# Optimization experiments

Hardware: AMD Instinct MI355X
Metric: run time of the kernel (lower is better)

## Reference

```python
import jax, jax.numpy as jnp
import numpy as np

HIDDEN = 1024
N_EMB = 4096
K_TOP = 64
EPS = 1e-6


def rmsnorm(x, w):
    xf = x.astype(jnp.float32)
    y = xf * jax.lax.rsqrt(jnp.mean(xf * xf, axis=-1, keepdims=True) + EPS)
    return y.astype(x.dtype) * w


def setup_inputs() -> dict:
    key = jax.random.key(0)
    ks = jax.random.split(key, 5)
    B, S, D, N = 16, 2048, HIDDEN, N_EMB
    bound = 1.0 / np.sqrt(D)  # torch Linear reset_parameters uniform bound
    return {
        "X": jax.random.normal(ks[0], (B, S, D), dtype=jnp.float32),
        "alpha": jnp.zeros((), dtype=jnp.float32),
        "E": jax.random.normal(ks[1], (N, D), dtype=jnp.float32) / np.sqrt(D),
        "Wq": jax.random.uniform(ks[2], (D, D), dtype=jnp.float32, minval=-bound, maxval=bound),
        "Wk": jax.random.uniform(ks[3], (D, D), dtype=jnp.float32, minval=-bound, maxval=bound),
        "xn_w": jnp.ones((D,), dtype=jnp.float32),
        "sn_w": jnp.ones((D,), dtype=jnp.float32),
        "on_w": jnp.ones((D,), dtype=jnp.float32),
    }


def reference(X, alpha, E, Wq, Wk, xn_w, sn_w, on_w):
    scale = HIDDEN ** (-0.5)
    Xn = rmsnorm(X, xn_w)            # (B,S,D)
    En = rmsnorm(E, sn_w)            # (N,D)
    Q = Xn @ Wq.T                    # (B,S,D)
    Km = En @ Wk.T                   # (N,D)
    scores = jnp.einsum('bsd,nd->bsn', Q, Km) * scale  # (B,S,N)
    global_scores = jnp.max(scores, axis=1)            # (B,N)
    top_vals, _ = jax.lax.top_k(global_scores, K_TOP)
    cutoff = top_vals[:, -1:]                          # (B,1)
    masked = jnp.where(global_scores >= cutoff, global_scores, -jnp.inf)
    dense_w = jax.nn.softmax(global_scores, axis=-1)
    sparse_w = jax.nn.softmax(masked, axis=-1)
    weights = alpha * dense_w + (1.0 - alpha) * sparse_w  # (B,N)
    O = rmsnorm(weights @ En, on_w)                      # (B,D)
    return O, weights
```

## Files before the change

kernel.cpp:

```cpp
#include <hip/hip_runtime.h>


namespace {

constexpr int D_DIM = 1024;
constexpr int NE    = 4096;
constexpr int BATCH = 16;
constexpr int SEQ   = 2048;
constexpr int MX    = BATCH * SEQ;
constexpr int KTOP  = 64;
constexpr int CAND  = 128;
constexpr int BK    = 32;

using f32x4  = __attribute__((ext_vector_type(4))) float;
using bf16x8 = __attribute__((ext_vector_type(8))) short;
using i32x4  = __attribute__((ext_vector_type(4))) int;

__device__ inline unsigned encf(float f) {
  unsigned u = __float_as_uint(f);
  return (u & 0x80000000u) ? ~u : (u | 0x80000000u);
}
__device__ inline float decf(unsigned e) {
  unsigned u = (e & 0x80000000u) ? (e ^ 0x80000000u) : ~e;
  return __uint_as_float(u);
}

__device__ inline unsigned short f2bf(float f) {
  unsigned u = __float_as_uint(f);
  unsigned lsb = (u >> 16) & 1u;
  u += 0x7fffu + lsb;
  return (unsigned short)(u >> 16);
}
__device__ inline float bf2f(unsigned short h) {
  return __uint_as_float(((unsigned)h) << 16);
}

__device__ inline void gload16(const void* gsrc, void* ldst) {
  __builtin_amdgcn_global_load_lds(
      (const __attribute__((address_space(1))) unsigned int*)gsrc,
      (__attribute__((address_space(3))) unsigned int*)ldst, 16, 0, 0);
}

__global__ void row_rinv_k(const float* __restrict__ X, float* __restrict__ rinv) {
  __shared__ float l4[4];
  int row = blockIdx.x;
  float4 v = ((const float4*)(X + (size_t)row * D_DIM))[threadIdx.x];
  float ss = v.x * v.x + v.y * v.y + v.z * v.z + v.w * v.w;
  for (int o = 32; o > 0; o >>= 1) ss += __shfl_xor(ss, o);
  int lane = threadIdx.x & 63, w = threadIdx.x >> 6;
  if (lane == 0) l4[w] = ss;
  __syncthreads();
  if (threadIdx.x == 0) {
    float t = l4[0] + l4[1] + l4[2] + l4[3];
    rinv[row] = rsqrtf(t * (1.0f / D_DIM) + 1e-6f);
  }
}

__global__ void rinv_quantx_k(const float* __restrict__ X, float* __restrict__ rinv,
                              float* __restrict__ sxr, int* __restrict__ XQ,
                              unsigned* __restrict__ gmax) {
  __shared__ float l4[4], m4[4];
  int row = blockIdx.x;
  if (row < 256) gmax[row * 256 + threadIdx.x] = 0u;
  float4 v = ((const float4*)(X + (size_t)row * D_DIM))[threadIdx.x];
  float ss = v.x * v.x + v.y * v.y + v.z * v.z + v.w * v.w;
  float am = fmaxf(fmaxf(fabsf(v.x), fabsf(v.y)), fmaxf(fabsf(v.z), fabsf(v.w)));
  for (int o = 32; o > 0; o >>= 1) {
    ss += __shfl_xor(ss, o);
    am = fmaxf(am, __shfl_xor(am, o));
  }
  int lane = threadIdx.x & 63, w = threadIdx.x >> 6;
  if (lane == 0) { l4[w] = ss; m4[w] = am; }
  __syncthreads();
  float t  = l4[0] + l4[1] + l4[2] + l4[3];
  float amax = fmaxf(fmaxf(m4[0], m4[1]), fmaxf(m4[2], m4[3]));
  amax = fmaxf(amax, 1e-30f);
  float ri = rsqrtf(t * (1.0f / D_DIM) + 1e-6f);
  if (threadIdx.x == 0) {
    rinv[row] = ri;
    sxr[row]  = ri * amax * (1.0f / 127.0f);
  }
  float qs = 127.0f / amax;
  int q0 = (int)rintf(v.x * qs) & 0xff;
  int q1 = (int)rintf(v.y * qs) & 0xff;
  int q2 = (int)rintf(v.z * qs) & 0xff;
  int q3 = (int)rintf(v.w * qs) & 0xff;
  XQ[(size_t)row * 256 + threadIdx.x] = q0 | (q1 << 8) | (q2 << 16) | (q3 << 24);
}

__global__ void prep_w_k(const float* __restrict__ Wq, const float* __restrict__ Wk,
                         const float* __restrict__ cw, float* __restrict__ T,
                         unsigned short* __restrict__ H, unsigned short* __restrict__ L) {
  __shared__ float t[32][33], u[32][33];
  int k0 = blockIdx.x * 32, d0 = blockIdx.y * 32;
  int tx = threadIdx.x & 31, ty4 = (threadIdx.x >> 5) * 4;
#pragma unroll
  for (int i = 0; i < 4; ++i) {
    t[ty4 + i][tx] = Wq[(size_t)(d0 + ty4 + i) * D_DIM + k0 + tx];
    u[ty4 + i][tx] = Wk[(size_t)(d0 + ty4 + i) * D_DIM + k0 + tx];
  }
  __syncthreads();
#pragma unroll
  for (int i = 0; i < 4; ++i) {
    int a = ty4 + i;
    T[(size_t)(k0 + a) * D_DIM + d0 + tx] = t[tx][a];
    float v = u[tx][a] * cw[k0 + a];
    unsigned short h = f2bf(v);
    H[(size_t)(k0 + a) * D_DIM + d0 + tx] = h;
    L[(size_t)(k0 + a) * D_DIM + d0 + tx] = f2bf(v - bf2f(h));
  }
}

template <int KLEN>
__global__ __launch_bounds__(256, 2) void gemm_a32_part_k(
    const float* __restrict__ A, const float* __restrict__ rinv,
    const unsigned short* __restrict__ BH, const unsigned short* __restrict__ BL,
    float* __restrict__ Of) {
  __shared__ __align__(16) float lA[128 * 32];
  __shared__ __align__(16) unsigned short lBH[128 * 32];
  __shared__ __align__(16) unsigned short lBL[128 * 32];
  __shared__ float ldsR[128];

  int tid = threadIdx.x;
  int lane = tid & 63, wid = tid >> 6;
  int wr = wid >> 1, wc = wid & 1;
  int fr = lane & 15, fg = lane >> 4;
  long m0 = (long)blockIdx.x * 128;
  long n0 = (long)blockIdx.y * 128;
  int kbeg = blockIdx.z * KLEN;
  float* Op = Of + (size_t)blockIdx.z * ((size_t)gridDim.x * 128 * D_DIM);

  if (tid < 128) ldsR[tid] = rinv ? rinv[m0 + tid] : 1.0f;

  f32x4 acc[4][4] = {};

  for (int kk = kbeg; kk < kbeg + KLEN; kk += BK) {
#pragma unroll
    for (int i = 0; i < 4; ++i) {
      int chunk = i * 256 + tid;
      int r = chunk >> 3, c = chunk & 7;
      int cs = c ^ (r & 7);
      const float* src = A + (m0 + r) * (long)D_DIM + kk + cs * 4;
      gload16(src, (void*)(lA + ((i * 256 + (tid & ~63)) << 2)));
    }
#pragma unroll
    for (int i = 0; i < 2; ++i) {
      int chunk = i * 256 + tid;
      int r = chunk >> 2, c = chunk & 3;
      int cs = c ^ ((r >> 1) & 3);
      long boff = (n0 + r) * (long)D_DIM + kk + cs * 8;
      int lo = (i * 256 + (tid & ~63)) << 3;
      gload16(BH + boff, (void*)(lBH + lo));
      gload16(BL + boff, (void*)(lBL + lo));
    }
    __syncthreads();

    bf16x8 aH[4], aL[4], bH[4], bL[4];
#pragma unroll
    for (int m = 0; m < 4; ++m) {
      int row = wr * 64 + m * 16 + fr;
      int rm = row & 7;
      f32x4 p0 = *(const f32x4*)(lA + row * 32 + (((fg * 2 + 0) ^ rm) * 4));
      f32x4 p1 = *(const f32x4*)(lA + row * 32 + (((fg * 2 + 1) ^ rm) * 4));
#pragma unroll
      for (int e = 0; e < 8; ++e) {
        float f = (e < 4) ? p0[e] : p1[e - 4];
        unsigned short h = f2bf(f);
        aH[m][e] = (short)h;
        aL[m][e] = (short)f2bf(f - bf2f(h));
      }
    }
#pragma unroll
    for (int n = 0; n < 4; ++n) {
      int row = wc * 64 + n * 16 + fr;
      int sc = fg ^ ((row >> 1) & 3);
      bH[n] = *(const bf16x8*)(lBH + row * 32 + sc * 8);
      bL[n] = *(const bf16x8*)(lBL + row * 32 + sc * 8);
    }
#pragma unroll
    for (int m = 0; m < 4; ++m)
#pragma unroll
      for (int n = 0; n < 4; ++n) {
        acc[m][n] = __builtin_amdgcn_mfma_f32_16x16x32_bf16(aH[m], bH[n], acc[m][n], 0, 0, 0);
        acc[m][n] = __builtin_amdgcn_mfma_f32_16x16x32_bf16(aH[m], bL[n], acc[m][n], 0, 0, 0);
        acc[m][n] = __builtin_amdgcn_mfma_f32_16x16x32_bf16(aL[m], bH[n], acc[m][n], 0, 0, 0);
      }
    __syncthreads();
  }

#pragma unroll
  for (int m = 0; m < 4; ++m) {
#pragma unroll
    for (int j = 0; j < 4; ++j) {
      int rloc = wr * 64 + m * 16 + fg * 4 + j;
      float rv = ldsR[rloc];
      long grow = m0 + rloc;
#pragma unroll
      for (int n = 0; n < 4; ++n) {
        long gcol = n0 + wc * 64 + n * 16 + fr;
        Op[grow * D_DIM + gcol] = acc[m][n][j] * rv;
      }
    }
  }
}

__global__ void sum_split_w2_k(const float* __restrict__ P0, const float* __restrict__ P1,
                               const float* __restrict__ P2, const float* __restrict__ P3,
                               unsigned short* __restrict__ H, unsigned short* __restrict__ L) {
  size_t i4 = ((size_t)blockIdx.x * 256 + threadIdx.x) * 4;
  float4 a = *(const float4*)(P0 + i4);
  float4 b = *(const float4*)(P1 + i4);
  float4 c = *(const float4*)(P2 + i4);
  float4 d = *(const float4*)(P3 + i4);
  float v[4] = {a.x + b.x + c.x + d.x, a.y + b.y + c.y + d.y,
                a.z + b.z + c.z + d.z, a.w + b.w + c.w + d.w};
  unsigned short h[4], l[4];
#pragma unroll
  for (int i = 0; i < 4; ++i) {
    h[i] = f2bf(v[i]);
    l[i] = f2bf(v[i] - bf2f(h[i]));
  }
  *(ushort4*)(H + i4) = make_ushort4(h[0], h[1], h[2], h[3]);
  *(ushort4*)(L + i4) = make_ushort4(l[0], l[1], l[2], l[3]);
}

__global__ void sum_split_p_k(const float* __restrict__ P0, const float* __restrict__ P1,
                              unsigned short* __restrict__ PH, unsigned short* __restrict__ PL,
                              float* __restrict__ sp, int* __restrict__ PQ) {
  __shared__ float m4[4];
  int row = blockIdx.x, tid = threadIdx.x;
  size_t i4 = (size_t)row * D_DIM + tid * 4;
  float4 a = *(const float4*)(P0 + i4);
  float4 b = *(const float4*)(P1 + i4);
  float v0 = a.x + b.x, v1 = a.y + b.y, v2 = a.z + b.z, v3 = a.w + b.w;
  unsigned short h0 = f2bf(v0), h1 = f2bf(v1), h2 = f2bf(v2), h3 = f2bf(v3);
  *(ushort4*)(PH + i4) = make_ushort4(h0, h1, h2, h3);
  *(ushort4*)(PL + i4) = make_ushort4(f2bf(v0 - bf2f(h0)), f2bf(v1 - bf2f(h1)),
                                      f2bf(v2 - bf2f(h2)), f2bf(v3 - bf2f(h3)));
  float am = fmaxf(fmaxf(fabsf(v0), fabsf(v1)), fmaxf(fabsf(v2), fabsf(v3)));
  for (int o = 32; o > 0; o >>= 1) am = fmaxf(am, __shfl_xor(am, o));
  int lane = tid & 63, w = tid >> 6;
  if (lane == 0) m4[w] = am;
  __syncthreads();
  float amax = fmaxf(fmaxf(m4[0], m4[1]), fmaxf(m4[2], m4[3]));
  amax = fmaxf(amax, 1e-30f);
  if (tid == 0) sp[row] = amax * (1.0f / 127.0f);
  float qs = 127.0f / amax;
  int q0 = (int)rintf(v0 * qs) & 0xff;
  int q1 = (int)rintf(v1 * qs) & 0xff;
  int q2 = (int)rintf(v2 * qs) & 0xff;
  int q3 = (int)rintf(v3 * qs) & 0xff;
  PQ[(size_t)row * 256 + tid] = q0 | (q1 << 8) | (q2 << 16) | (q3 << 24);
}

__global__ __launch_bounds__(512, 4) void gemm_scores1_k(
    const signed char* __restrict__ XQ, const signed char* __restrict__ PQ,
    const float* __restrict__ sxr, const float* __restrict__ sp,
    unsigned* __restrict__ gmax) {
  __shared__ __align__(16) signed char lA[3][128 * 64];
  __shared__ __align__(16) signed char lB[3][256 * 64];
  __shared__ float ldsR[128];

  int tid = threadIdx.x;
  int lane = tid & 63, wid = tid >> 6;
  int wwr = wid >> 2;
  int wwc = wid & 3;
  int fr = lane & 15, fg = lane >> 4;

  int id = blockIdx.x;
  int xcd = id & 7;
  int r = id >> 3;
  int tile_n = (r & 7) | ((r >> 8) << 3);
  int tile_m = xcd * 32 + ((r >> 3) & 31);
  long m0 = (long)tile_m * 128;
  long n0 = (long)tile_n * 256;

  if (tid < 128) ldsR[tid] = sxr[m0 + tid];

  auto stageTile = [&](int buf, int kt) {
    int kk = kt * 64;
    {
      int r2 = tid >> 2, c = tid & 3;
      int cs = c ^ ((r2 >> 1) & 3);
      gload16(XQ + (m0 + r2) * (long)D_DIM + kk + cs * 16,
              (void*)(&lA[buf][0] + ((tid & ~63) << 4)));
    }
#pragma unroll
    for (int i = 0; i < 2; ++i) {
      int chunk = i * 512 + tid;
      int r2 = chunk >> 2, c = chunk & 3;
      int cs = c ^ ((r2 >> 1) & 3);
      gload16(PQ + (n0 + r2) * (long)D_DIM + kk + cs * 16,
              (void*)(&lB[buf][0] + ((i * 512 + (tid & ~63)) << 4)));
    }
  };

  i32x4 acc[4][4] = {};

  stageTile(0, 0);
  stageTile(1, 1);
  asm volatile("s_waitcnt lgkmcnt(0)" ::: "memory");

#pragma unroll
  for (int kt = 0; kt < 16; ++kt) {
    const int cur = kt % 3;
    const int nxt = (kt + 2) % 3;
    const signed char* As = &lA[cur][0];
    const signed char* Bs = &lB[cur][0];

    if (kt < 15) {
      asm volatile("s_waitcnt vmcnt(3)" ::: "memory");
    } else {
      asm volatile("s_waitcnt vmcnt(0)" ::: "memory");
    }
    __builtin_amdgcn_s_barrier();
    if (kt + 2 < 16) stageTile(nxt, kt + 2);

    i32x4 aF[4], bF[4];
#pragma unroll
    for (int mi = 0; mi < 4; ++mi) {
      int row = wwr * 64 + mi * 16 + fr;
      int ck = fg ^ ((row >> 1) & 3);
      aF[mi] = *(const i32x4*)(As + row * 64 + ck * 16);
    }
#pragma unroll
    for (int ni = 0; ni < 4; ++ni) {
      int row = wwc * 64 + ni * 16 + fr;
      int ck = fg ^ ((row >> 1) & 3);
      bF[ni] = *(const i32x4*)(Bs + row * 64 + ck * 16);
    }
    __builtin_amdgcn_s_setprio(1);
#pragma unroll
    for (int mi = 0; mi < 4; ++mi)
#pragma unroll
      for (int ni = 0; ni < 4; ++ni)
        acc[mi][ni] = __builtin_amdgcn_mfma_i32_16x16x64_i8(
            aF[mi], bF[ni], acc[mi][ni], 0, 0, 0);
    __builtin_amdgcn_s_setprio(0);
  }

  int b = (int)(m0 >> 11);
#pragma unroll
  for (int ni = 0; ni < 4; ++ni) {
    long col = n0 + wwc * 64 + ni * 16 + fr;
    float spc = sp[col];
    float v = -3.0e38f;
#pragma unroll
    for (int mi = 0; mi < 4; ++mi)
#pragma unroll
      for (int j = 0; j < 4; ++j) {
        int row = wwr * 64 + mi * 16 + fg * 4 + j;
        v = fmaxf(v, (float)acc[mi][ni][j] * ldsR[row]);
      }
    v *= spc;
    v = fmaxf(v, __shfl_xor(v, 16));
    v = fmaxf(v, __shfl_xor(v, 32));
    if (fg == 0) {
      atomicMax(&gmax[(long)b * NE + col], encf(v * 0.03125f));
    }
  }
}

__global__ void cand_select_k(const unsigned* __restrict__ gmax,
                              int* __restrict__ candIdx, unsigned* __restrict__ gmax2) {
  __shared__ unsigned enc[NE];
  __shared__ int ic[257];
  int tid = threadIdx.x;
  int lane = tid & 63, w = tid >> 6;
  int zb = blockIdx.x;
  if (tid < CAND) gmax2[zb * CAND + tid] = 0u;
  const unsigned* g = gmax + (size_t)zb * NE;
  for (int i = tid; i < NE; i += 256) enc[i] = g[i];
  __syncthreads();

  unsigned cur = 0;
  for (int bit = 31; bit >= 0; --bit) {
    unsigned cand = cur | (1u << bit);
    int c = 0;
    for (int i = tid; i < NE; i += 256) c += (enc[i] >= cand) ? 1 : 0;
    for (int o = 32; o > 0; o >>= 1) c += __shfl_xor(c, o);
    __syncthreads();
    if (lane == 0) ic[w] = c;
    __syncthreads();
    int tot = ic[0] + ic[1] + ic[2] + ic[3];
    if (tot >= CAND) cur = cand;
    if (tot == CAND) break;
  }

  int myc = 0;
  for (int i = tid; i < NE; i += 256) myc += (enc[i] >= cur) ? 1 : 0;
  __syncthreads();
  ic[tid] = myc;
  __syncthreads();
  if (tid == 0) {
    int s = 0;
    for (int t = 0; t < 256; ++t) { int v = ic[t]; ic[t] = s; s += v; }
  }
  __syncthreads();
  int off = ic[tid];
  for (int i = tid; i < NE; i += 256)
    if (enc[i] >= cur) {
      if (off < CAND) candIdx[zb * CAND + off] = i;
      ++off;
    }
}

__global__ __launch_bounds__(256, 2) void gemm_rescore_k(
    const float* __restrict__ X, const float* __restrict__ rinvA,
    const unsigned short* __restrict__ PH, const unsigned short* __restrict__ PL,
    const int* __restrict__ candIdx, unsigned* __restrict__ gmax2) {
  __shared__ __align__(16) float lA[128 * 32];
  __shared__ __align__(16) unsigned short lBH[128 * 32], lBL[128 * 32];
  __shared__ float ldsR[128];

  int tid = threadIdx.x;
  int lane = tid & 63, wid = tid >> 6;
  int wr = wid >> 1, wc = wid & 1;
  int fr = lane & 15, fg = lane >> 4;
  int z = blockIdx.z;
  long m0 = (long)blockIdx.x * 128;
  long arow0 = (long)z * SEQ + m0;

  if (tid < 128) ldsR[tid] = rinvA[arow0 + tid];

  long bbase[2];
#pragma unroll
  for (int i = 0; i < 2; ++i) {
    int r = (i * 256 + tid) >> 2;
    bbase[i] = (long)candIdx[z * CAND + r] * D_DIM;
  }

  f32x4 acc[4][4] = {};

  for (int kk = 0; kk < D_DIM; kk += BK) {
#pragma unroll
    for (int i = 0; i < 4; ++i) {
      int chunk = i * 256 + tid;
      int r = chunk >> 3, c = chunk & 7;
      int cs = c ^ (r & 7);
      const float* src = X + (arow0 + r) * (long)D_DIM + kk + cs * 4;
      gload16(src, (void*)(lA + ((i * 256 + (tid & ~63)) << 2)));
    }
#pragma unroll
    for (int i = 0; i < 2; ++i) {
      int chunk = i * 256 + tid;
      int c = chunk & 3;
      int r = chunk >> 2;
      int cs = c ^ ((r >> 1) & 3);
      long boff = bbase[i] + kk + cs * 8;
      int lo = (i * 256 + (tid & ~63)) << 3;
      gload16(PH + boff, (void*)(lBH + lo));
      gload16(PL + boff, (void*)(lBL + lo));
    }
    __syncthreads();

    bf16x8 aH[4], aL[4], bH[4], bL[4];
#pragma unroll
    for (int m = 0; m < 4; ++m) {
      int row = wr * 64 + m * 16 + fr;
      int rm = row & 7;
      f32x4 p0 = *(const f32x4*)(lA + row * 32 + (((fg * 2 + 0) ^ rm) * 4));
      f32x4 p1 = *(const f32x4*)(lA + row * 32 + (((fg * 2 + 1) ^ rm) * 4));
#pragma unroll
      for (int e = 0; e < 8; ++e) {
        float f = (e < 4) ? p0[e] : p1[e - 4];
        unsigned short h = f2bf(f);
        aH[m][e] = (short)h;
        aL[m][e] = (short)f2bf(f - bf2f(h));
      }
    }
#pragma unroll
    for (int n = 0; n < 4; ++n) {
      int row = wc * 64 + n * 16 + fr;
      int sc = fg ^ ((row >> 1) & 3);
      bH[n] = *(const bf16x8*)(lBH + row * 32 + sc * 8);
      bL[n] = *(const bf16x8*)(lBL + row * 32 + sc * 8);
    }
#pragma unroll
    for (int m = 0; m < 4; ++m)
#pragma unroll
      for (int n = 0; n < 4; ++n) {
        acc[m][n] = __builtin_amdgcn_mfma_f32_16x16x32_bf16(aH[m], bH[n], acc[m][n], 0, 0, 0);
        acc[m][n] = __builtin_amdgcn_mfma_f32_16x16x32_bf16(aH[m], bL[n], acc[m][n], 0, 0, 0);
        acc[m][n] = __builtin_amdgcn_mfma_f32_16x16x32_bf16(aL[m], bH[n], acc[m][n], 0, 0, 0);
      }
    __syncthreads();
  }

#pragma unroll
  for (int n = 0; n < 4; ++n) {
    float v = -3.0e38f;
#pragma unroll
    for (int m = 0; m < 4; ++m)
#pragma unroll
      for (int j = 0; j < 4; ++j) {
        float rv = ldsR[wr * 64 + m * 16 + fg * 4 + j];
        v = fmaxf(v, acc[m][n][j] * rv);
      }
    v = fmaxf(v, __shfl_xor(v, 16));
    v = fmaxf(v, __shfl_xor(v, 32));
    if (fg == 0) {
      int col = wc * 64 + n * 16 + fr;
      atomicMax(&gmax2[z * CAND + col], encf(v * 0.03125f));
    }
  }
}

__global__ void final_k(const unsigned* __restrict__ gmax,
                        const unsigned* __restrict__ gmax2,
                        const int* __restrict__ candIdx,
                        const float* __restrict__ alpha_p,
                        const float* __restrict__ E, const float* __restrict__ rinvE,
                        const float* __restrict__ sn_w, const float* __restrict__ on_w,
                        float* __restrict__ wout, float* __restrict__ O) {
  __shared__ unsigned enc[NE];
  __shared__ int sel[NE];
  __shared__ unsigned ubc[4];
  __shared__ float l4[4];
  __shared__ int ic[257];
  int tid = threadIdx.x;
  int lane = tid & 63, w = tid >> 6;
  int b = blockIdx.x;
  const unsigned* g = gmax + (size_t)b * NE;
  for (int i = tid; i < NE; i += 256) enc[i] = g[i];
  __syncthreads();
  if (tid < CAND) enc[candIdx[b * CAND + tid]] = gmax2[b * CAND + tid];
  __syncthreads();

  unsigned mx = 0;
  for (int i = tid; i < NE; i += 256) mx = enc[i] > mx ? enc[i] : mx;
  for (int o = 32; o > 0; o >>= 1) {
    unsigned other = (unsigned)__shfl_xor((int)mx, o);
    if (other > mx) mx = other;
  }
  if (lane == 0) ubc[w] = mx;
  __syncthreads();
  unsigned m1e = ubc[0];
  for (int t = 1; t < 4; ++t) m1e = ubc[t] > m1e ? ubc[t] : m1e;
  float m1 = decf(m1e);

  unsigned cur = 0;
  for (int bit = 31; bit >= 0; --bit) {
    unsigned cand = cur | (1u << bit);
    int c = 0;
    for (int i = tid; i < NE; i += 256) c += (enc[i] >= cand) ? 1 : 0;
    for (int o = 32; o > 0; o >>= 1) c += __shfl_xor(c, o);
    __syncthreads();
    if (lane == 0) ic[w] = c;
    __syncthreads();
    int tot = ic[0] + ic[1] + ic[2] + ic[3];
    if (tot >= KTOP) cur = cand;
    if (tot == KTOP) break;
  }

  float sd = 0.f, ssum = 0.f;
  for (int i = tid; i < NE; i += 256) {
    float e = expf(decf(enc[i]) - m1);
    sd += e;
    if (enc[i] >= cur) ssum += e;
  }
  for (int o = 32; o > 0; o >>= 1) { sd += __shfl_xor(sd, o); ssum += __shfl_xor(ssum, o); }
  __syncthreads();
  if (lane == 0) { l4[w] = sd; }
  __syncthreads();
  float SD = l4[0] + l4[1] + l4[2] + l4[3];
  __syncthreads();
  if (lane == 0) { l4[w] = ssum; }
  __syncthreads();
  float SS = l4[0] + l4[1] + l4[2] + l4[3];

  float alpha = alpha_p[0];
  float wd = alpha / SD;
  float ws_ = (1.0f - alpha) / SS;
  for (int i = tid; i < NE; i += 256) {
    float e = expf(decf(enc[i]) - m1);
    float wv = wd * e + ((enc[i] >= cur) ? ws_ * e : 0.0f);
    wout[(size_t)b * NE + i] = wv;
  }

  int myc = 0;
  for (int i = tid; i < NE; i += 256) myc += (enc[i] >= cur) ? 1 : 0;
  __syncthreads();
  ic[tid] = myc;
  __syncthreads();
  if (tid == 0) {
    int s = 0;
    for (int t = 0; t < 256; ++t) { int v = ic[t]; ic[t] = s; s += v; }
    ic[256] = s;
  }
  __syncthreads();
  int off = ic[tid];
  for (int i = tid; i < NE; i += 256)
    if (enc[i] >= cur) sel[off++] = i;
  __syncthreads();
  int nsel = ic[256];

  float acc[4] = {0.f, 0.f, 0.f, 0.f};
  if (alpha == 0.0f) {
    float coef = wd + ws_;
    for (int j = 0; j < nsel; ++j) {
      int n = sel[j];
      float e = expf(decf(enc[n]) - m1);
      float wv = coef * e * rinvE[n];
      const float* er = E + (size_t)n * D_DIM;
#pragma unroll
      for (int i = 0; i < 4; ++i) acc[i] += wv * er[tid + 256 * i];
    }
  } else {
    for (int n = 0; n < NE; ++n) {
      float e = expf(decf(enc[n]) - m1);
      float wv = (wd * e + ((enc[n] >= cur) ? ws_ * e : 0.0f)) * rinvE[n];
      const float* er = E + (size_t)n * D_DIM;
#pragma unroll
      for (int i = 0; i < 4; ++i) acc[i] += wv * er[tid + 256 * i];
    }
  }
  float ssq = 0.f;
#pragma unroll
  for (int i = 0; i < 4; ++i) {
    acc[i] *= sn_w[tid + 256 * i];
    ssq += acc[i] * acc[i];
  }
  for (int o = 32; o > 0; o >>= 1) ssq += __shfl_xor(ssq, o);
  if (lane == 0) l4[w] = ssq;
  __syncthreads();
  float tot = l4[0] + l4[1] + l4[2] + l4[3];
  float rn = rsqrtf(tot * (1.0f / D_DIM) + 1e-6f);
#pragma unroll
  for (int i = 0; i < 4; ++i)
    O[(size_t)b * D_DIM + tid + 256 * i] = acc[i] * rn * on_w[tid + 256 * i];
}

}

extern "C" void kernel_launch(void* const* d_in, const int* in_sizes, int n_in,
                              void* d_out, int out_size, void* d_ws, size_t ws_size,
                              hipStream_t stream) {
  const float* X     = (const float*)d_in[0];
  const float* alpha = (const float*)d_in[1];
  const float* E     = (const float*)d_in[2];
  const float* Wq    = (const float*)d_in[3];
  const float* Wk    = (const float*)d_in[4];
  const float* xn_w  = (const float*)d_in[5];
  const float* sn_w  = (const float*)d_in[6];
  const float* on_w  = (const float*)d_in[7];
  float* O    = (float*)d_out;
  float* Wout = (float*)d_out + (size_t)BATCH * D_DIM;

  char* ws = (char*)d_ws;
  size_t off = 0;
  auto alloc = [&](size_t bytes) {
    char* p = ws + off;
    off += (bytes + 255) & ~(size_t)255;
    return p;
  };
  signed char*    XQ    = (signed char*)alloc((size_t)MX * D_DIM);
  signed char*    PQ    = (signed char*)alloc((size_t)NE * D_DIM);
  float*          WqTf  = (float*)alloc((size_t)D_DIM * D_DIM * 4);
  unsigned short* WkTH  = (unsigned short*)alloc((size_t)D_DIM * D_DIM * 2);
  unsigned short* WkTL  = (unsigned short*)alloc((size_t)D_DIM * D_DIM * 2);
  unsigned short* W2TH  = (unsigned short*)alloc((size_t)D_DIM * D_DIM * 2);
  unsigned short* W2TL  = (unsigned short*)alloc((size_t)D_DIM * D_DIM * 2);
  unsigned short* PH    = (unsigned short*)alloc((size_t)NE * D_DIM * 2);
  unsigned short* PL    = (unsigned short*)alloc((size_t)NE * D_DIM * 2);
  float*          W2p   = (float*)alloc((size_t)4 * D_DIM * D_DIM * 4);
  float*          Pp    = (float*)alloc((size_t)2 * NE * D_DIM * 4);
  float* rinvX = (float*)alloc((size_t)MX * 4);
  float* sxr   = (float*)alloc((size_t)MX * 4);
  float* rinvE = (float*)alloc((size_t)NE * 4);
  float* sp    = (float*)alloc((size_t)NE * 4);
  unsigned* gmax  = (unsigned*)alloc((size_t)BATCH * NE * 4);
  unsigned* gmax2 = (unsigned*)alloc((size_t)BATCH * CAND * 4);
  int* candIdx = (int*)alloc((size_t)BATCH * CAND * 4);
  if (off > ws_size) return;

  row_rinv_k<<<NE, 256, 0, stream>>>(E, rinvE);
  prep_w_k<<<dim3(D_DIM / 32, D_DIM / 32), 256, 0, stream>>>(
      Wq, Wk, sn_w, WqTf, WkTH, WkTL);
  gemm_a32_part_k<256><<<dim3(8, 8, 4), 256, 0, stream>>>(
      WqTf, xn_w, WkTH, WkTL, W2p);
  sum_split_w2_k<<<D_DIM * D_DIM / 1024, 256, 0, stream>>>(
      W2p, W2p + (size_t)D_DIM * D_DIM, W2p + (size_t)2 * D_DIM * D_DIM,
      W2p + (size_t)3 * D_DIM * D_DIM, W2TH, W2TL);
  gemm_a32_part_k<512><<<dim3(NE / 128, D_DIM / 128, 2), 256, 0, stream>>>(
      E, rinvE, W2TH, W2TL, Pp);
  sum_split_p_k<<<NE, 256, 0, stream>>>(
      Pp, Pp + (size_t)NE * D_DIM, PH, PL, sp, (int*)PQ);

  rinv_quantx_k<<<MX, 256, 0, stream>>>(X, rinvX, sxr, (int*)XQ, gmax);
  gemm_scores1_k<<<(MX / 128) * (NE / 256), 512, 0, stream>>>(XQ, PQ, sxr, sp, gmax);

  cand_select_k<<<BATCH, 256, 0, stream>>>(gmax, candIdx, gmax2);
  gemm_rescore_k<<<dim3(SEQ / 128, 1, BATCH), 256, 0, stream>>>(
      X, rinvX, PH, PL, candIdx, gmax2);
  final_k<<<BATCH, 256, 0, stream>>>(gmax, gmax2, candIdx, alpha, E, rinvE,
                                     sn_w, on_w, Wout, O);
}
```

Before: 375.7 us.

## Fold candidate selection into rescore and final kernels, dropping cand_select launch

Removes the separate cand_select_k launch. Each gemm_rescore_k block (16 per batch) and final_k now recompute the radix-select of the 128 candidates from gmax in LDS. gmax2 zeroing moves into rinv_quantx_k. This saves one kernel launch and its serialization gap, at the cost of redundant selection work in every rescore block and 16KB of extra LDS, which may reduce occupancy of the rescore GEMM.

After: 390.7 us. +4.0%, slower.

```diff
diff --git a/kernel.cpp b/kernel.cpp
--- a/kernel.cpp
+++ b/kernel.cpp
@@ -41,6 +41,42 @@
       (__attribute__((address_space(3))) unsigned int*)ldst, 16, 0, 0);
 }
 
+__device__ inline unsigned derive_cands(const unsigned* enc, int* ic,
+                                        int* candL, int tid) {
+  int lane = tid & 63, w = tid >> 6;
+  unsigned cur = 0;
+  for (int bit = 31; bit >= 0; --bit) {
+    unsigned cand = cur | (1u << bit);
+    int c = 0;
+    for (int i = tid; i < NE; i += 256) c += (enc[i] >= cand) ? 1 : 0;
+    for (int o = 32; o > 0; o >>= 1) c += __shfl_xor(c, o);
+    __syncthreads();
+    if (lane == 0) ic[w] = c;
+    __syncthreads();
+    int tot = ic[0] + ic[1] + ic[2] + ic[3];
+    if (tot >= CAND) cur = cand;
+    if (tot == CAND) break;
+  }
+  int myc = 0;
+  for (int i = tid; i < NE; i += 256) myc += (enc[i] >= cur) ? 1 : 0;
+  __syncthreads();
+  ic[tid] = myc;
+  __syncthreads();
+  if (tid == 0) {
+    int s = 0;
+    for (int t = 0; t < 256; ++t) { int v = ic[t]; ic[t] = s; s += v; }
+  }
+  __syncthreads();
+  int off = ic[tid];
+  for (int i = tid; i < NE; i += 256)
+    if (enc[i] >= cur) {
+      if (off < CAND) candL[off] = i;
+      ++off;
+    }
+  __syncthreads();
+  return cur;
+}
+
 __global__ void row_rinv_k(const float* __restrict__ X, float* __restrict__ rinv) {
   __shared__ float l4[4];
   int row = blockIdx.x;
@@ -58,10 +94,11 @@
 
 __global__ void rinv_quantx_k(const float* __restrict__ X, float* __restrict__ rinv,
                               float* __restrict__ sxr, int* __restrict__ XQ,
-                              unsigned* __restrict__ gmax) {
+                              unsigned* __restrict__ gmax, unsigned* __restrict__ gmax2) {
   __shared__ float l4[4], m4[4];
   int row = blockIdx.x;
   if (row < 256) gmax[row * 256 + threadIdx.x] = 0u;
+  else if (row < 264) gmax2[(row - 256) * 256 + threadIdx.x] = 0u;
   float4 v = ((const float4*)(X + (size_t)row * D_DIM))[threadIdx.x];
   float ss = v.x * v.x + v.y * v.y + v.z * v.z + v.w * v.w;
   float am = fmaxf(fmaxf(fabsf(v.x), fabsf(v.y)), fmaxf(fabsf(v.z), fabsf(v.w)));
@@ -361,57 +398,16 @@
   }
 }
 
-__global__ void cand_select_k(const unsigned* __restrict__ gmax,
-                              int* __restrict__ candIdx, unsigned* __restrict__ gmax2) {
-  __shared__ unsigned enc[NE];
-  __shared__ int ic[257];
-  int tid = threadIdx.x;
-  int lane = tid & 63, w = tid >> 6;
-  int zb = blockIdx.x;
-  if (tid < CAND) gmax2[zb * CAND + tid] = 0u;
-  const unsigned* g = gmax + (size_t)zb * NE;
-  for (int i = tid; i < NE; i += 256) enc[i] = g[i];
-  __syncthreads();
-
-  unsigned cur = 0;
-  for (int bit = 31; bit >= 0; --bit) {
-    unsigned cand = cur | (1u << bit);
-    int c = 0;
-    for (int i = tid; i < NE; i += 256) c += (enc[i] >= cand) ? 1 : 0;
-    for (int o = 32; o > 0; o >>= 1) c += __shfl_xor(c, o);
-    __syncthreads();
-    if (lane == 0) ic[w] = c;
-    __syncthreads();
-    int tot = ic[0] + ic[1] + ic[2] + ic[3];
-    if (tot >= CAND) cur = cand;
-    if (tot == CAND) break;
-  }
-
-  int myc = 0;
-  for (int i = tid; i < NE; i += 256) myc += (enc[i] >= cur) ? 1 : 0;
-  __syncthreads();
-  ic[tid] = myc;
-  __syncthreads();
-  if (tid == 0) {
-    int s = 0;
-    for (int t = 0; t < 256; ++t) { int v = ic[t]; ic[t] = s; s += v; }
-  }
-  __syncthreads();
-  int off = ic[tid];
-  for (int i = tid; i < NE; i += 256)
-    if (enc[i] >= cur) {
-      if (off < CAND) candIdx[zb * CAND + off] = i;
-      ++off;
-    }
-}
-
 __global__ __launch_bounds__(256, 2) void gemm_rescore_k(
     const float* __restrict__ X, const float* __restrict__ rinvA,
     const unsigned short* __restrict__ PH, const unsigned short* __restrict__ PL,
-    const int* __restrict__ candIdx, unsigned* __restrict__ gmax2) {
+    const unsigned* __restrict__ gmax, unsigned* __restrict__ gmax2) {
   __shared__ __align__(16) float lA[128 * 32];
   __shared__ __align__(16) unsigned short lBH[128 * 32], lBL[128 * 32];
   __shared__ float ldsR[128];
+  __shared__ unsigned enc[NE];
+  __shared__ int ic[256];
+  __shared__ int candL[CAND];
 
   int tid = threadIdx.x;
   int lane = tid & 63, wid = tid >> 6;
@@ -423,11 +419,16 @@
 
   if (tid < 128) ldsR[tid] = rinvA[arow0 + tid];
 
+  const unsigned* g = gmax + (size_t)z * NE;
+  for (int i = tid; i < NE; i += 256) enc[i] = g[i];
+  __syncthreads();
+  derive_cands(enc, ic, candL, tid);
+
   long bbase[2];
 #pragma unroll
   for (int i = 0; i < 2; ++i) {
     int r = (i * 256 + tid) >> 2;
-    bbase[i] = (long)candIdx[z * CAND + r] * D_DIM;
+    bbase[i] = (long)candL[r] * D_DIM;
   }
 
   f32x4 acc[4][4] = {};
@@ -508,7 +509,6 @@
 
 __global__ void final_k(const unsigned* __restrict__ gmax,
                         const unsigned* __restrict__ gmax2,
-                        const int* __restrict__ candIdx,
                         const float* __restrict__ alpha_p,
                         const float* __restrict__ E, const float* __restrict__ rinvE,
                         const float* __restrict__ sn_w, const float* __restrict__ on_w,
@@ -518,13 +518,16 @@
   __shared__ unsigned ubc[4];
   __shared__ float l4[4];
   __shared__ int ic[257];
+  __shared__ int candL[CAND];
   int tid = threadIdx.x;
   int lane = tid & 63, w = tid >> 6;
   int b = blockIdx.x;
   const unsigned* g = gmax + (size_t)b * NE;
   for (int i = tid; i < NE; i += 256) enc[i] = g[i];
   __syncthreads();
-  if (tid < CAND) enc[candIdx[b * CAND + tid]] = gmax2[b * CAND + tid];
+
+  derive_cands(enc, ic, candL, tid);
+  if (tid < CAND) enc[candL[tid]] = gmax2[b * CAND + tid];
   __syncthreads();
 
   unsigned mx = 0;
@@ -671,7 +674,6 @@
   float* sp    = (float*)alloc((size_t)NE * 4);
   unsigned* gmax  = (unsigned*)alloc((size_t)BATCH * NE * 4);
   unsigned* gmax2 = (unsigned*)alloc((size_t)BATCH * CAND * 4);
-  int* candIdx = (int*)alloc((size_t)BATCH * CAND * 4);
   if (off > ws_size) return;
 
   row_rinv_k<<<NE, 256, 0, stream>>>(E, rinvE);
@@ -687,12 +689,11 @@
   sum_split_p_k<<<NE, 256, 0, stream>>>(
       Pp, Pp + (size_t)NE * D_DIM, PH, PL, sp, (int*)PQ);
 
-  rinv_quantx_k<<<MX, 256, 0, stream>>>(X, rinvX, sxr, (int*)XQ, gmax);
+  rinv_quantx_k<<<MX, 256, 0, stream>>>(X, rinvX, sxr, (int*)XQ, gmax, gmax2);
   gemm_scores1_k<<<(MX / 128) * (NE / 256), 512, 0, stream>>>(XQ, PQ, sxr, sp, gmax);
 
-  cand_select_k<<<BATCH, 256, 0, stream>>>(gmax, candIdx, gmax2);
   gemm_rescore_k<<<dim3(SEQ / 128, 1, BATCH), 256, 0, stream>>>(
-      X, rinvX, PH, PL, candIdx, gmax2);
-  final_k<<<BATCH, 256, 0, stream>>>(gmax, gmax2, candIdx, alpha, E, rinvE,
+      X, rinvX, PH, PL, gmax, gmax2);
+  final_k<<<BATCH, 256, 0, stream>>>(gmax, gmax2, alpha, E, rinvE,
                                      sn_w, on_w, Wout, O);
 }
```
